# Optimization experiments

Measured on AMD Instinct MI355X. Metric: run time of the kernel, lower is better.

Reference implementation:

```python
import jax, jax.numpy as jnp
import numpy as np

ITEM_NUM = 100000
EMBED = 128
HIDDEN = 256
BETA = 0.5
B, H = 2048, 200


def setup_inputs() -> dict:
    key = jax.random.key(0)
    ks = jax.random.split(key, 10)
    history = jax.random.randint(ks[0], (B, H), 0, ITEM_NUM)
    target = jax.random.randint(ks[1], (B,), 0, ITEM_NUM)
    history_region = jax.random.randint(ks[2], (B, H), 0, 64)
    target_region = jax.random.randint(ks[3], (B,), 0, 64)
    # scaled small since forward multiplies by 1000 before sigmoid
    target_distance = jax.random.uniform(ks[4], (B, H, 2), dtype=jnp.float32) * 1e-3
    embed_history = 0.01 * jax.random.normal(ks[5], (ITEM_NUM, EMBED), dtype=jnp.float32)
    embed_target = 0.01 * jax.random.normal(ks[6], (ITEM_NUM, EMBED), dtype=jnp.float32)
    W1 = 0.05 * jax.random.normal(ks[7], (EMBED + 2, HIDDEN), dtype=jnp.float32)
    b1 = jnp.zeros((HIDDEN,), dtype=jnp.float32)
    W2 = 0.05 * jax.random.normal(ks[8], (HIDDEN, 1), dtype=jnp.float32)
    Wd = 0.5 * jax.random.normal(ks[9], (2, 2), dtype=jnp.float32)
    bd = jnp.zeros((2,), dtype=jnp.float32)
    return {"history": history, "target": target, "history_region": history_region,
            "target_region": target_region, "target_distance": target_distance,
            "embed_history": embed_history, "embed_target": embed_target,
            "W1": W1, "b1": b1, "W2": W2, "Wd": Wd, "bd": bd}


def reference(history, target, history_region, target_region, target_distance,
              embed_history, embed_target, W1, b1, W2, Wd, bd):
    h = embed_history[history]                 # [B,H,d]
    t = embed_target[target]                   # [B,d]
    # dist_layer: sigmoid(Linear(2,2)(1000 * lat_long))
    dist = jax.nn.sigmoid((target_distance * 1000.0) @ Wd + bd)   # [B,H,2]
    inp = jnp.concatenate([h * t[:, None, :], dist], axis=-1)     # [B,H,d+2]
    attn = jax.nn.relu(inp @ W1 + b1) @ W2                        # [B,H,1]
    mask = (history != target[:, None]).astype(h.dtype)
    exp_A = jnp.exp(attn[..., 0]) * mask                          # [B,H]
    exp_sum = jnp.sum(exp_A, axis=-1, keepdims=True) ** BETA      # [B,1]
    w = exp_A / exp_sum                                           # [B,H]
    pred = jnp.einsum('bhd,bh,bd->b', h, w, t)                    # [B]
    return jax.nn.sigmoid(pred)
```

## Files before the change

kernel.cpp:

```cpp
#include <hip/hip_runtime.h>
#include <hip/hip_bf16.h>

#define B_SZ 2048
#define H_SZ 200
#define EMB 128
#define HID 256

typedef short bf16x8 __attribute__((ext_vector_type(8)));
typedef float f32x4 __attribute__((ext_vector_type(4)));

#define WAIT_VM(n) asm volatile("s_waitcnt vmcnt(" #n ")" ::: "memory")
#define WAIT_LGKM  asm volatile("s_waitcnt lgkmcnt(0)" ::: "memory")
#define BAR        asm volatile("s_barrier" ::: "memory")

__device__ __forceinline__ unsigned short bfc(float x) {
    unsigned u = __float_as_uint(x);
    u += 0x7FFFu + ((u >> 16) & 1u);
    return (unsigned short)(u >> 16);
}
__device__ __forceinline__ float bf2f(unsigned short h) {
    return __uint_as_float(((unsigned)h) << 16);
}

__global__ void prep_w1t(const float* __restrict__ W1, unsigned short* __restrict__ W1TB) {
    int i = blockIdx.x * 256 + threadIdx.x;
    int n = i >> 7;
    int k = i & 127;
    W1TB[i] = bfc(W1[k * HID + n]);
}

__global__ void prep_ehb(const float* __restrict__ eh, unsigned short* __restrict__ ehb) {
    size_t t = (size_t)blockIdx.x * 256 + threadIdx.x;
    const float4* src = (const float4*)eh + t * 2;
    float4 a = src[0], b = src[1];
    uint4 o;
    o.x = (unsigned)bfc(a.x) | ((unsigned)bfc(a.y) << 16);
    o.y = (unsigned)bfc(a.z) | ((unsigned)bfc(a.w) << 16);
    o.z = (unsigned)bfc(b.x) | ((unsigned)bfc(b.y) << 16);
    o.w = (unsigned)bfc(b.z) | ((unsigned)bfc(b.w) << 16);
    ((uint4*)ehb)[t] = o;
}

__device__ __forceinline__ void gld_lds16(const unsigned short* g, unsigned short* l) {
    __builtin_amdgcn_global_load_lds(
        (const __attribute__((address_space(1))) void*)(g),
        (__attribute__((address_space(3))) void*)(l),
        16, 0, 0);
}

__global__ __launch_bounds__(512, 4) void attn_kernel(
    const int* __restrict__ history, const int* __restrict__ target,
    const float* __restrict__ td, const unsigned short* __restrict__ ehb,
    const float* __restrict__ et, const unsigned short* __restrict__ W1TB,
    const float* __restrict__ b1, const float* __restrict__ W2,
    const float* __restrict__ W1, const float* __restrict__ Wd,
    const float* __restrict__ bd, float* __restrict__ out)
{
    __shared__ __align__(16) unsigned short Abuf[4][64][128];
    __shared__ float red[4][64][9];
    __shared__ float2 dpack[256];
    __shared__ int idxs[256];
    __shared__ float t_f32[EMB];
    __shared__ float finred[16];

    const int tid = threadIdx.x;
    const int b   = blockIdx.x;
    const int tgt = target[b];

    if (tid < 128) t_f32[tid] = et[(size_t)tgt * EMB + tid];
    {
        const int m0 = tid - 128;
        if (m0 >= 0 && m0 < H_SZ) {
            const int row = b * H_SZ + m0;
            idxs[m0] = history[row];
            float x0 = td[(size_t)row * 2 + 0] * 1000.f;
            float x1 = td[(size_t)row * 2 + 1] * 1000.f;
            float d0 = x0 * Wd[0] + x1 * Wd[2] + bd[0];
            float d1 = x0 * Wd[1] + x1 * Wd[3] + bd[1];
            d0 = 1.f / (1.f + expf(-d0));
            d1 = 1.f / (1.f + expf(-d1));
            dpack[m0] = make_float2(d0, d1);
        } else if (m0 >= H_SZ && m0 < 128 + 128) {
            if (m0 < 256) dpack[m0] = make_float2(0.f, 0.f);
        }
    }
    WAIT_LGKM; BAR;

    const int l  = tid & 63;
    const int w  = tid >> 6;
    const int lr = l & 15;
    const int lq = l >> 4;

    bf16x8 bfrB[2][4];
    float b1v[2], w2v[2], wd0[2], wd1[2];
#pragma unroll
    for (int nt = 0; nt < 2; ++nt) {
        const int n = w * 32 + nt * 16 + lr;
        b1v[nt] = b1[n];
        w2v[nt] = W2[n];
        wd0[nt] = W1[128 * HID + n];
        wd1[nt] = W1[129 * HID + n];
#pragma unroll
        for (int ks = 0; ks < 4; ++ks) {
            const int k0 = ks * 32 + lq * 8;
            bf16x8 wv = *reinterpret_cast<const bf16x8*>(W1TB + n * EMB + k0);
            bf16x8 o;
#pragma unroll
            for (int j = 0; j < 8; ++j) {
                float f = bf2f((unsigned short)wv[j]) * t_f32[k0 + j];
                o[j] = (short)bfc(f);
            }
            bfrB[nt][ks] = o;
        }
    }

    WAIT_VM(0);

#pragma unroll
    for (int t = 0; t < 3; ++t) {
#pragma unroll
        for (int j = 0; j < 2; ++j) {
            const int rd = w * 8 + j * 4 + (l >> 4);
            const int cc = (l & 15) ^ (rd & 7);
            const unsigned short* g = ehb + (size_t)idxs[t * 64 + rd] * EMB + cc * 8;
            gld_lds16(g, &Abuf[t][w * 8 + j * 4][0]);
        }
    }
#pragma unroll
    for (int j = 0; j < 2; ++j) {
        const int rd = j * 4 + (l >> 4);
        const int cc = (l & 15) ^ (rd & 7);
        const unsigned short* g = ehb + (size_t)idxs[192 + rd] * EMB + cc * 8;
        gld_lds16(g, &Abuf[3][j * 4][0]);
    }

#pragma unroll
    for (int t = 0; t < 4; ++t) {
        if (t == 0)      WAIT_VM(6);
        else if (t == 1) WAIT_VM(4);
        else if (t == 2) WAIT_VM(2);
        else             WAIT_VM(0);
        WAIT_LGKM;
        BAR;

        const int mc = (t == 3) ? 1 : 4;
        const unsigned short* A = &Abuf[t][0][0];

        f32x4 acc[4][2];
#pragma unroll
        for (int mt = 0; mt < 4; ++mt)
#pragma unroll
            for (int nt = 0; nt < 2; ++nt)
                acc[mt][nt] = (f32x4){0.f, 0.f, 0.f, 0.f};

#pragma unroll
        for (int ks = 0; ks < 4; ++ks) {
#pragma unroll
            for (int mt = 0; mt < 4; ++mt) if (mt < mc) {
                const int ar = mt * 16 + lr;
                const bf16x8 af = *reinterpret_cast<const bf16x8*>(
                    A + ar * EMB + (((ks * 4 + lq) ^ (ar & 7)) * 8));
                acc[mt][0] = __builtin_amdgcn_mfma_f32_16x16x32_bf16(af, bfrB[0][ks], acc[mt][0], 0, 0, 0);
                acc[mt][1] = __builtin_amdgcn_mfma_f32_16x16x32_bf16(af, bfrB[1][ks], acc[mt][1], 0, 0, 0);
            }
        }

#pragma unroll
        for (int mt = 0; mt < 4; ++mt) if (mt < mc) {
#pragma unroll
            for (int r = 0; r < 4; ++r) {
                const int mrow = mt * 16 + lq * 4 + r;
                float2 d = dpack[t * 64 + mrow];
                float s = 0.f;
#pragma unroll
                for (int nt = 0; nt < 2; ++nt) {
                    float hv = acc[mt][nt][r] + b1v[nt] + d.x * wd0[nt] + d.y * wd1[nt];
                    hv = fmaxf(hv, 0.f);
                    s += hv * w2v[nt];
                }
                s += __shfl_xor(s, 1);
                s += __shfl_xor(s, 2);
                s += __shfl_xor(s, 4);
                s += __shfl_xor(s, 8);
                if (lr == 0) red[t][mrow][w] = s;
            }
        }
    }

    WAIT_LGKM; BAR;

    float se = 0.f, su = 0.f;
    if (tid < H_SZ) {
        const int tt = tid >> 6, mrow = tid & 63;
        float attn = 0.f;
#pragma unroll
        for (int ww = 0; ww < 8; ++ww) attn += red[tt][mrow][ww];
        const unsigned short* Arow = &Abuf[tt][mrow][0];
        float u = 0.f;
#pragma unroll
        for (int c = 0; c < 16; ++c) {
            bf16x8 hv = *reinterpret_cast<const bf16x8*>(Arow + ((c ^ (mrow & 7)) * 8));
#pragma unroll
            for (int j = 0; j < 8; ++j)
                u += bf2f((unsigned short)hv[j]) * t_f32[c * 8 + j];
        }
        float e = (idxs[tid] != tgt) ? expf(attn) : 0.f;
        se = e;
        su = e * u;
    }
#pragma unroll
    for (int off = 1; off < 64; off <<= 1) {
        se += __shfl_xor(se, off);
        su += __shfl_xor(su, off);
    }
    if (l == 0) { finred[w * 2] = se; finred[w * 2 + 1] = su; }
    WAIT_LGKM; BAR;
    if (tid == 0) {
        float SE = 0.f, SU = 0.f;
#pragma unroll
        for (int ww = 0; ww < 8; ++ww) { SE += finred[2 * ww]; SU += finred[2 * ww + 1]; }
        out[b] = 1.f / (1.f + expf(-SU / sqrtf(SE)));
    }
}

extern "C" void kernel_launch(void* const* d_in, const int* in_sizes, int n_in,
                              void* d_out, int out_size, void* d_ws, size_t ws_size,
                              hipStream_t stream) {
    const int*   history = (const int*)d_in[0];
    const int*   target  = (const int*)d_in[1];
    const float* td      = (const float*)d_in[4];
    const float* eh      = (const float*)d_in[5];
    const float* et      = (const float*)d_in[6];
    const float* W1      = (const float*)d_in[7];
    const float* b1      = (const float*)d_in[8];
    const float* W2      = (const float*)d_in[9];
    const float* Wd      = (const float*)d_in[10];
    const float* bd      = (const float*)d_in[11];
    float* out = (float*)d_out;

    char* ws = (char*)d_ws;
    unsigned short* W1TB = (unsigned short*)ws;
    unsigned short* ehb  = (unsigned short*)(ws + 65536);

    prep_w1t<<<HID * EMB / 256, 256, 0, stream>>>(W1, W1TB);
    prep_ehb<<<1600000 / 256, 256, 0, stream>>>(eh, ehb);
    attn_kernel<<<B_SZ, 512, 0, stream>>>(history, target, td, ehb, et, W1TB,
                                          b1, W2, W1, Wd, bd, out);
}
```

Measured before the change: 109.8 us.

## Fold distance features into MFMA K-step, swap operands, parallelize u dot product

Pads W1 to K=160 so the two distance features enter the MFMA as a fifth K slice instead of per-element FMAs. The A and B operands are swapped so each lane holds four consecutive hidden units, which lets the ReLU·W2 reduction use two cross-lane shuffles instead of four per row. Issues the embedding gather before building the weight fragments, so the gather overlaps weight loading. The h·t dot product is spread across all threads per tile rather than done serially by 200 threads at the end. In exchange the distance values and the target vector are rounded to bf16, which slightly reduces precision.

```diff
diff --git a/kernel.cpp b/kernel.cpp
--- a/kernel.cpp
+++ b/kernel.cpp
@@ -5,6 +5,7 @@
 #define H_SZ 200
 #define EMB 128
 #define HID 256
+#define KW 160
 
 typedef short bf16x8 __attribute__((ext_vector_type(8)));
 typedef float f32x4 __attribute__((ext_vector_type(4)));
@@ -24,9 +25,10 @@
 
 __global__ void prep_w1t(const float* __restrict__ W1, unsigned short* __restrict__ W1TB) {
     int i = blockIdx.x * 256 + threadIdx.x;
-    int n = i >> 7;
-    int k = i & 127;
-    W1TB[i] = bfc(W1[k * HID + n]);
+    int n = i / KW;
+    int k = i - n * KW;
+    float v = (k < 130) ? W1[k * HID + n] : 0.f;
+    W1TB[i] = bfc(v);
 }
 
 __global__ void prep_ehb(const float* __restrict__ eh, unsigned short* __restrict__ ehb) {
@@ -53,24 +55,29 @@
     const float* __restrict__ td, const unsigned short* __restrict__ ehb,
     const float* __restrict__ et, const unsigned short* __restrict__ W1TB,
     const float* __restrict__ b1, const float* __restrict__ W2,
-    const float* __restrict__ W1, const float* __restrict__ Wd,
-    const float* __restrict__ bd, float* __restrict__ out)
+    const float* __restrict__ Wd, const float* __restrict__ bd,
+    float* __restrict__ out)
 {
     __shared__ __align__(16) unsigned short Abuf[4][64][128];
     __shared__ float red[4][64][9];
-    __shared__ float2 dpack[256];
+    __shared__ unsigned Adist[256];
     __shared__ int idxs[256];
     __shared__ float t_f32[EMB];
-    __shared__ float finred[16];
+    __shared__ __align__(16) unsigned short tbf[EMB];
+    __shared__ float u_arr[256];
+    __shared__ float finred[8];
 
     const int tid = threadIdx.x;
     const int b   = blockIdx.x;
     const int tgt = target[b];
 
-    if (tid < 128) t_f32[tid] = et[(size_t)tgt * EMB + tid];
-    {
+    if (tid < 128) {
+        float tf = et[(size_t)tgt * EMB + tid];
+        t_f32[tid] = tf;
+        tbf[tid] = bfc(tf);
+    } else if (tid < 384) {
         const int m0 = tid - 128;
-        if (m0 >= 0 && m0 < H_SZ) {
+        if (m0 < H_SZ) {
             const int row = b * H_SZ + m0;
             idxs[m0] = history[row];
             float x0 = td[(size_t)row * 2 + 0] * 1000.f;
@@ -79,9 +86,9 @@
             float d1 = x0 * Wd[1] + x1 * Wd[3] + bd[1];
             d0 = 1.f / (1.f + expf(-d0));
             d1 = 1.f / (1.f + expf(-d1));
-            dpack[m0] = make_float2(d0, d1);
-        } else if (m0 >= H_SZ && m0 < 128 + 128) {
-            if (m0 < 256) dpack[m0] = make_float2(0.f, 0.f);
+            Adist[m0] = (unsigned)bfc(d0) | ((unsigned)bfc(d1) << 16);
+        } else {
+            Adist[m0] = 0u;
         }
     }
     WAIT_LGKM; BAR;
@@ -91,48 +98,45 @@
     const int lr = l & 15;
     const int lq = l >> 4;
 
-    bf16x8 bfrB[2][4];
-    float b1v[2], w2v[2], wd0[2], wd1[2];
+#pragma unroll
+    for (int t = 0; t < 3; ++t) {
+#pragma unroll
+        for (int j = 0; j < 2; ++j) {
+            const int rd = w * 8 + j * 4 + lq;
+            const int cc = lr ^ (rd & 7);
+            gld_lds16(ehb + (size_t)idxs[t * 64 + rd] * EMB + cc * 8,
+                      &Abuf[t][w * 8 + j * 4][0]);
+        }
+    }
+#pragma unroll
+    for (int j = 0; j < 2; ++j) {
+        const int rd = j * 4 + lq;
+        const int cc = lr ^ (rd & 7);
+        gld_lds16(ehb + (size_t)idxs[192 + rd] * EMB + cc * 8, &Abuf[3][j * 4][0]);
+    }
+
+    bf16x8 bfrA[2][5];
+    f32x4 b1v[2], w2v[2];
 #pragma unroll
     for (int nt = 0; nt < 2; ++nt) {
         const int n = w * 32 + nt * 16 + lr;
-        b1v[nt] = b1[n];
-        w2v[nt] = W2[n];
-        wd0[nt] = W1[128 * HID + n];
-        wd1[nt] = W1[129 * HID + n];
+        b1v[nt] = *reinterpret_cast<const f32x4*>(b1 + w * 32 + nt * 16 + lq * 4);
+        w2v[nt] = *reinterpret_cast<const f32x4*>(W2 + w * 32 + nt * 16 + lq * 4);
 #pragma unroll
         for (int ks = 0; ks < 4; ++ks) {
-            const int k0 = ks * 32 + lq * 8;
-            bf16x8 wv = *reinterpret_cast<const bf16x8*>(W1TB + n * EMB + k0);
+            bf16x8 wv = *reinterpret_cast<const bf16x8*>(W1TB + n * KW + ks * 32 + lq * 8);
             bf16x8 o;
 #pragma unroll
-            for (int j = 0; j < 8; ++j) {
-                float f = bf2f((unsigned short)wv[j]) * t_f32[k0 + j];
-                o[j] = (short)bfc(f);
-            }
-            bfrB[nt][ks] = o;
-        }
-    }
-
-    WAIT_VM(0);
-
-#pragma unroll
-    for (int t = 0; t < 3; ++t) {
-#pragma unroll
-        for (int j = 0; j < 2; ++j) {
-            const int rd = w * 8 + j * 4 + (l >> 4);
-            const int cc = (l & 15) ^ (rd & 7);
-            const unsigned short* g = ehb + (size_t)idxs[t * 64 + rd] * EMB + cc * 8;
-            gld_lds16(g, &Abuf[t][w * 8 + j * 4][0]);
-        }
-    }
-#pragma unroll
-    for (int j = 0; j < 2; ++j) {
-        const int rd = j * 4 + (l >> 4);
-        const int cc = (l & 15) ^ (rd & 7);
-        const unsigned short* g = ehb + (size_t)idxs[192 + rd] * EMB + cc * 8;
-        gld_lds16(g, &Abuf[3][j * 4][0]);
-    }
+            for (int j = 0; j < 8; ++j)
+                o[j] = (short)bfc(bf2f((unsigned short)wv[j]) * t_f32[ks * 32 + lq * 8 + j]);
+            bfrA[nt][ks] = o;
+        }
+        bfrA[nt][4] = *reinterpret_cast<const bf16x8*>(W1TB + n * KW + 128 + lq * 8);
+    }
+
+    const int uo = tid & 7, um = tid >> 3;
+    const bf16x8 tbu0 = *reinterpret_cast<const bf16x8*>(tbf + (2 * uo) * 8);
+    const bf16x8 tbu1 = *reinterpret_cast<const bf16x8*>(tbf + (2 * uo + 1) * 8);
 
 #pragma unroll
     for (int t = 0; t < 4; ++t) {
@@ -140,11 +144,9 @@
         else if (t == 1) WAIT_VM(4);
         else if (t == 2) WAIT_VM(2);
         else             WAIT_VM(0);
-        WAIT_LGKM;
         BAR;
 
         const int mc = (t == 3) ? 1 : 4;
-        const unsigned short* A = &Abuf[t][0][0];
 
         f32x4 acc[4][2];
 #pragma unroll
@@ -154,71 +156,78 @@
                 acc[mt][nt] = (f32x4){0.f, 0.f, 0.f, 0.f};
 
 #pragma unroll
-        for (int ks = 0; ks < 4; ++ks) {
+        for (int ks = 0; ks < 5; ++ks) {
 #pragma unroll
             for (int mt = 0; mt < 4; ++mt) if (mt < mc) {
                 const int ar = mt * 16 + lr;
-                const bf16x8 af = *reinterpret_cast<const bf16x8*>(
-                    A + ar * EMB + (((ks * 4 + lq) ^ (ar & 7)) * 8));
-                acc[mt][0] = __builtin_amdgcn_mfma_f32_16x16x32_bf16(af, bfrB[0][ks], acc[mt][0], 0, 0, 0);
-                acc[mt][1] = __builtin_amdgcn_mfma_f32_16x16x32_bf16(af, bfrB[1][ks], acc[mt][1], 0, 0, 0);
+                bf16x8 af;
+                if (ks < 4) {
+                    af = *reinterpret_cast<const bf16x8*>(
+                        &Abuf[t][ar][(((ks * 4 + lq) ^ (ar & 7)) * 8)]);
+                } else {
+                    uint4 tv4 = make_uint4((lq == 0) ? Adist[t * 64 + ar] : 0u, 0u, 0u, 0u);
+                    af = *reinterpret_cast<bf16x8*>(&tv4);
+                }
+#pragma unroll
+                for (int nt = 0; nt < 2; ++nt)
+                    acc[mt][nt] = __builtin_amdgcn_mfma_f32_16x16x32_bf16(
+                        bfrA[nt][ks], af, acc[mt][nt], 0, 0, 0);
             }
         }
 
+        {
+            const unsigned short* Ar = &Abuf[t][um][0];
+            bf16x8 h0 = *reinterpret_cast<const bf16x8*>(Ar + (((2 * uo)     ^ (um & 7)) * 8));
+            bf16x8 h1 = *reinterpret_cast<const bf16x8*>(Ar + (((2 * uo + 1) ^ (um & 7)) * 8));
+            float ua = 0.f;
+#pragma unroll
+            for (int j = 0; j < 8; ++j) {
+                ua += bf2f((unsigned short)h0[j]) * bf2f((unsigned short)tbu0[j]);
+                ua += bf2f((unsigned short)h1[j]) * bf2f((unsigned short)tbu1[j]);
+            }
+            ua += __shfl_xor(ua, 1);
+            ua += __shfl_xor(ua, 2);
+            ua += __shfl_xor(ua, 4);
+            if (uo == 0) u_arr[t * 64 + um] = ua;
+        }
+
 #pragma unroll
         for (int mt = 0; mt < 4; ++mt) if (mt < mc) {
-#pragma unroll
-            for (int r = 0; r < 4; ++r) {
-                const int mrow = mt * 16 + lq * 4 + r;
-                float2 d = dpack[t * 64 + mrow];
-                float s = 0.f;
-#pragma unroll
-                for (int nt = 0; nt < 2; ++nt) {
-                    float hv = acc[mt][nt][r] + b1v[nt] + d.x * wd0[nt] + d.y * wd1[nt];
-                    hv = fmaxf(hv, 0.f);
-                    s += hv * w2v[nt];
-                }
-                s += __shfl_xor(s, 1);
-                s += __shfl_xor(s, 2);
-                s += __shfl_xor(s, 4);
-                s += __shfl_xor(s, 8);
-                if (lr == 0) red[t][mrow][w] = s;
-            }
+            float s = 0.f;
+#pragma unroll
+            for (int nt = 0; nt < 2; ++nt)
+#pragma unroll
+                for (int r = 0; r < 4; ++r)
+                    s += fmaxf(acc[mt][nt][r] + b1v[nt][r], 0.f) * w2v[nt][r];
+            s += __shfl_xor(s, 16);
+            s += __shfl_xor(s, 32);
+            if (l < 16) red[t][mt * 16 + l][w] = s;
         }
     }
 
     WAIT_LGKM; BAR;
 
-    float se = 0.f, su = 0.f;
-    if (tid < H_SZ) {
-        const int tt = tid >> 6, mrow = tid & 63;
+    if (tid < 256) {
+        const int tt = tid >> 6, mr = tid & 63;
         float attn = 0.f;
 #pragma unroll
-        for (int ww = 0; ww < 8; ++ww) attn += red[tt][mrow][ww];
-        const unsigned short* Arow = &Abuf[tt][mrow][0];
-        float u = 0.f;
-#pragma unroll
-        for (int c = 0; c < 16; ++c) {
-            bf16x8 hv = *reinterpret_cast<const bf16x8*>(Arow + ((c ^ (mrow & 7)) * 8));
-#pragma unroll
-            for (int j = 0; j < 8; ++j)
-                u += bf2f((unsigned short)hv[j]) * t_f32[c * 8 + j];
-        }
-        float e = (idxs[tid] != tgt) ? expf(attn) : 0.f;
-        se = e;
-        su = e * u;
-    }
-#pragma unroll
-    for (int off = 1; off < 64; off <<= 1) {
-        se += __shfl_xor(se, off);
-        su += __shfl_xor(su, off);
-    }
-    if (l == 0) { finred[w * 2] = se; finred[w * 2 + 1] = su; }
+        for (int ww = 0; ww < 8; ++ww) attn += red[tt][mr][ww];
+        const bool valid = (tid < H_SZ) && (idxs[tid] != tgt);
+        float e  = valid ? expf(attn) : 0.f;
+        float se = e;
+        float su = valid ? e * u_arr[tid] : 0.f;
+#pragma unroll
+        for (int off = 1; off < 64; off <<= 1) {
+            se += __shfl_xor(se, off);
+            su += __shfl_xor(su, off);
+        }
+        if (l == 0) { finred[w * 2] = se; finred[w * 2 + 1] = su; }
+    }
     WAIT_LGKM; BAR;
     if (tid == 0) {
         float SE = 0.f, SU = 0.f;
 #pragma unroll
-        for (int ww = 0; ww < 8; ++ww) { SE += finred[2 * ww]; SU += finred[2 * ww + 1]; }
+        for (int ww = 0; ww < 4; ++ww) { SE += finred[2 * ww]; SU += finred[2 * ww + 1]; }
         out[b] = 1.f / (1.f + expf(-SU / sqrtf(SE)));
     }
 }
@@ -240,10 +249,10 @@
 
     char* ws = (char*)d_ws;
     unsigned short* W1TB = (unsigned short*)ws;
-    unsigned short* ehb  = (unsigned short*)(ws + 65536);
-
-    prep_w1t<<<HID * EMB / 256, 256, 0, stream>>>(W1, W1TB);
+    unsigned short* ehb  = (unsigned short*)(ws + 81920);
+
+    prep_w1t<<<HID * KW / 256, 256, 0, stream>>>(W1, W1TB);
     prep_ehb<<<1600000 / 256, 256, 0, stream>>>(eh, ehb);
     attn_kernel<<<B_SZ, 512, 0, stream>>>(history, target, td, ehb, et, W1TB,
-                                          b1, W2, W1, Wd, bd, out);
-}
+                                          b1, W2, Wd, bd, out);
+}
```

Result: slower. 145.1 us (+32.1%).
